# Optimization experiments

Hardware: AMD Instinct MI355X
Metric: run time of the kernel (lower is better)

## Reference

```python
import jax, jax.numpy as jnp
import numpy as np

B, C, M, K, V, D, H, A, L, HF = 2, 128, 4, 4, 64, 1024, 16, 64, 4, 2048
E = M + K
EPS = 1e-5
THETA = 10000.0


def _rmsnorm(x, w):
    return x * jax.lax.rsqrt(jnp.mean(x * x, -1, keepdims=True) + EPS) * w


def _l2norm(x):
    n = jnp.sqrt(jnp.sum(x * x, -1, keepdims=True))
    return x / jnp.maximum(n, EPS)


def _rope(x, cos, sin):
    x1, x2 = jnp.split(x, 2, axis=-1)
    return jnp.concatenate([x1 * cos + x2 * sin, -x1 * sin + x2 * cos], -1)


def _forward(x_input, dec_w1, dec_w2, pos_emb, Wqkv, Wo, Wup, Wdown, attn_norm_w, ffn_norm_w, doc):
    b = x_input.shape[0]
    c = x_input.shape[1] // M
    # decoder_w1 then 'b (c m) (k v) -> b c k (m v)', decoder_w2, pos emb
    x = jnp.einsum('bsd,od->bso', x_input, dec_w1)
    x = x.reshape(b, c, M, K, V).transpose(0, 1, 3, 2, 4).reshape(b, c, K, M * V)
    x = jnp.einsum('bcku,du->bckd', x, dec_w2) + pos_emb
    # decoder_include_original_token: prepend original m tokens per block
    x = jnp.concatenate([x_input.reshape(b, c, M, D), x], axis=2).reshape(b, c * E, D)
    s = c * E
    # mask_mod (decoder_global_original_attn): (causal & kv%e<k & same_doc) | same_block
    idx = jnp.arange(s)
    blk = idx // E
    docs = doc[:, blk]  # [b, s]
    doc_m = docs[:, :, None] == docs[:, None, :]
    causal = blk[:, None] >= blk[None, :]
    kv_ok = (idx % E) < K
    same = blk[:, None] == blk[None, :]
    mask = (causal[None] & kv_ok[None, None, :] & doc_m) | same[None]  # [b, s, s]
    # rotary tables (applied post head-split, dim A)
    inv_freq = (1.0 / THETA) ** (jnp.arange(0, A, 2) / A)
    freqs = jnp.arange(s)[:, None] * inv_freq[None, :]
    cos, sin = jnp.cos(freqs), jnp.sin(freqs)  # [s, A/2]
    scale = 1.0 / jnp.sqrt(jnp.float32(A))
    neg = jnp.float32(-1e30)

    def heads(t):
        return t.reshape(b, s, H, A).transpose(0, 2, 1, 3)

    for li in range(L):
        xn = _rmsnorm(x, attn_norm_w[li])
        qkv = jnp.einsum('bsd,od->bso', xn, Wqkv[li])
        q, k, v = jnp.split(qkv, 3, axis=-1)
        q, k, v = heads(q), heads(k), heads(v)
        q, k = _l2norm(q), _l2norm(k)  # qk_norm
        q, k = _rope(q, cos, sin), _rope(k, cos, sin)
        scores = jnp.einsum('bhqa,bhka->bhqk', q, k) * scale
        scores = jnp.where(mask[:, None], scores, neg)
        probs = jax.nn.softmax(scores, axis=-1)
        attn = jnp.einsum('bhqk,bhka->bhqa', probs, v)
        attn = attn.transpose(0, 2, 1, 3).reshape(b, s, D)
        x1_in = jnp.einsum('bsd,od->bso', attn, Wo[li]) + x
        xf = _rmsnorm(x1_in, ffn_norm_w[li])
        up = jnp.einsum('bsd,od->bso', xf, Wup[li])
        u1, u2 = jnp.split(up, 2, axis=-1)
        x = jnp.einsum('bsh,dh->bsd', jax.nn.silu(u1) * u2, Wdown[li]) + x1_in
    # 'b (c e) d -> (b c) e d' then drop original tokens
    return x.reshape(b * c, E, D)[:, M:]


def setup_inputs() -> dict:
    key = jax.random.key(0)
    ks = jax.random.split(key, 10)
    sc = 0.02
    return {
        'x_input': jax.random.normal(ks[0], (B, C * M, D), jnp.float32),
        'doc': jnp.sort(jax.random.randint(ks[1], (B, C), 0, 4), axis=-1),
        'dec_w1': jax.random.normal(ks[2], (K * V, D), jnp.float32) * sc,
        'dec_w2': jax.random.normal(ks[3], (D, M * V), jnp.float32) * sc,
        'pos_emb': jax.random.normal(ks[4], (1, 1, K, D), jnp.float32) * sc,
        'Wqkv': jax.random.normal(ks[5], (L, 3 * D, D), jnp.float32) * sc,
        'Wo': jax.random.normal(ks[6], (L, D, D), jnp.float32) * sc,
        'Wup': jax.random.normal(ks[7], (L, 2 * HF, D), jnp.float32) * sc,
        'Wdown': jax.random.normal(ks[8], (L, D, HF), jnp.float32) * sc,
        'attn_norm_w': jnp.ones((L, D), jnp.float32),
        'ffn_norm_w': jnp.ones((L, D), jnp.float32),
    }


def reference(x_input, doc, dec_w1, dec_w2, pos_emb, Wqkv, Wo, Wup, Wdown, attn_norm_w, ffn_norm_w):
    return _forward(x_input, dec_w1, dec_w2, pos_emb, Wqkv, Wo, Wup, Wdown, attn_norm_w, ffn_norm_w, doc)
```

## Files before the change

kernel.cpp:

```cpp
#include <hip/hip_runtime.h>
#include <hip/hip_bf16.h>

typedef __bf16 bf16;
typedef __bf16 bf16x8 __attribute__((ext_vector_type(8)));
typedef __bf16 bf16x4 __attribute__((ext_vector_type(4)));
typedef float  f32x4  __attribute__((ext_vector_type(4)));

#define MFMA16(a, b, c) __builtin_amdgcn_mfma_f32_16x16x32_bf16(a, b, c, 0, 0, 0)

template <int EPI, int AF32, int BF32, int TM, int TN, int SK = 1>
__global__ __launch_bounds__(256 * SK) void gemm_bt(
    const void* __restrict__ Av, const void* __restrict__ Bv,
    const float* __restrict__ Res, void* __restrict__ Out,
    int Ntot, int Ktot, int lda)
{
    constexpr int PA = TM / 64, PB = TN / 64;
    constexpr int WN = (TN == 128) ? ((TM == 128) ? 2 : 4) : 2;
    constexpr int WM = 4 / WN;
    constexpr int I = TM / (WM * 16), J = TN / (WN * 16);
    __shared__ __align__(16) bf16 As[2][SK][TM][40];
    __shared__ __align__(16) bf16 Bs[2][SK][TN][40];
    static_assert(SK == 1 || sizeof(As) >= TM * TN * 4, "combine buffer fits in As");
    const int tid  = threadIdx.x;
    const int grp  = (SK > 1) ? (tid >> 8) : 0;
    const int t8   = tid & 255;
    const int wave = t8 >> 6, lane = tid & 63;
    const int quad = lane >> 4, l16 = lane & 15;
    const int wm = wave / WN, wn = wave % WN;
    const int rowW = wm * (TM / WM), colW = wn * (TN / WN);
    const int rowBase = blockIdx.y * TM, colBase = blockIdx.x * TN;

    f32x4 acc[I][J];
    const f32x4 z4 = {0.f, 0.f, 0.f, 0.f};
#pragma unroll
    for (int i = 0; i < I; i++)
#pragma unroll
        for (int j = 0; j < J; j++) acc[i][j] = z4;

    float4 rAf[PA][2]; bf16x8 rAb[PA];
    float4 rBf[PB][2]; bf16x8 rBb[PB];

    auto loadTile = [&](int kt) {
#pragma unroll
        for (int p = 0; p < PA; p++) {
            int ch = p * 256 + t8, r = ch >> 2, c8 = (ch & 3) << 3;
            if (AF32) {
                const float* s = (const float*)Av + (size_t)(rowBase + r) * lda + kt + c8;
                rAf[p][0] = *(const float4*)s; rAf[p][1] = *(const float4*)(s + 4);
            } else {
                rAb[p] = *(const bf16x8*)((const bf16*)Av + (size_t)(rowBase + r) * lda + kt + c8);
            }
        }
#pragma unroll
        for (int p = 0; p < PB; p++) {
            int ch = p * 256 + t8, r = ch >> 2, c8 = (ch & 3) << 3;
            if (BF32) {
                const float* s = (const float*)Bv + (size_t)(colBase + r) * Ktot + kt + c8;
                rBf[p][0] = *(const float4*)s; rBf[p][1] = *(const float4*)(s + 4);
            } else {
                rBb[p] = *(const bf16x8*)((const bf16*)Bv + (size_t)(colBase + r) * Ktot + kt + c8);
            }
        }
    };
    auto storeTile = [&](int buf) {
#pragma unroll
        for (int p = 0; p < PA; p++) {
            int ch = p * 256 + t8, r = ch >> 2, c8 = (ch & 3) << 3;
            bf16x8 t;
            if (AF32) {
                t[0]=(bf16)rAf[p][0].x; t[1]=(bf16)rAf[p][0].y; t[2]=(bf16)rAf[p][0].z; t[3]=(bf16)rAf[p][0].w;
                t[4]=(bf16)rAf[p][1].x; t[5]=(bf16)rAf[p][1].y; t[6]=(bf16)rAf[p][1].z; t[7]=(bf16)rAf[p][1].w;
            } else t = rAb[p];
            *(bf16x8*)&As[buf][grp][r][c8] = t;
        }
#pragma unroll
        for (int p = 0; p < PB; p++) {
            int ch = p * 256 + t8, r = ch >> 2, c8 = (ch & 3) << 3;
            bf16x8 t;
            if (BF32) {
                t[0]=(bf16)rBf[p][0].x; t[1]=(bf16)rBf[p][0].y; t[2]=(bf16)rBf[p][0].z; t[3]=(bf16)rBf[p][0].w;
                t[4]=(bf16)rBf[p][1].x; t[5]=(bf16)rBf[p][1].y; t[6]=(bf16)rBf[p][1].z; t[7]=(bf16)rBf[p][1].w;
            } else t = rBb[p];
            *(bf16x8*)&Bs[buf][grp][r][c8] = t;
        }
    };

    const int Kgrp  = Ktot / SK;
    const int kbase = grp * Kgrp;
    loadTile(kbase);
    storeTile(0);
    __syncthreads();
    const int nk = Kgrp >> 5;
    for (int k = 0; k < nk; k++) {
        const bool more = (k + 1) < nk;
        if (more) loadTile(kbase + ((k + 1) << 5));
        const int buf = k & 1;
        bf16x8 af[I], bfr[J];
#pragma unroll
        for (int i = 0; i < I; i++)
            af[i] = *(const bf16x8*)&As[buf][grp][rowW + i * 16 + l16][quad * 8];
#pragma unroll
        for (int j = 0; j < J; j++)
            bfr[j] = *(const bf16x8*)&Bs[buf][grp][colW + j * 16 + l16][quad * 8];
#pragma unroll
        for (int i = 0; i < I; i++)
#pragma unroll
            for (int j = 0; j < J; j++)
                acc[i][j] = MFMA16(af[i], bfr[j], acc[i][j]);
        if (more) { storeTile(buf ^ 1); __syncthreads(); }
    }

    if (SK == 2) {
        __syncthreads();
        float* red = (float*)&As[0][0][0][0];
        if (grp == 1) {
#pragma unroll
            for (int i = 0; i < I; i++)
#pragma unroll
                for (int j = 0; j < J; j++)
#pragma unroll
                    for (int r = 0; r < 4; r++)
                        red[(rowW + i * 16 + quad * 4 + r) * TN +
                            (colW + j * 16 + l16)] = acc[i][j][r];
        }
        __syncthreads();
        if (grp != 0) return;
#pragma unroll
        for (int i = 0; i < I; i++)
#pragma unroll
            for (int j = 0; j < J; j++)
#pragma unroll
                for (int r = 0; r < 4; r++)
                    acc[i][j][r] += red[(rowW + i * 16 + quad * 4 + r) * TN +
                                        (colW + j * 16 + l16)];
    }

#pragma unroll
    for (int i = 0; i < I; i++) {
        int row0 = rowBase + rowW + i * 16 + quad * 4;
#pragma unroll
        for (int j = 0; j < J; j++) {
            int col = colBase + colW + j * 16 + l16;
#pragma unroll
            for (int r = 0; r < 4; r++) {
                size_t off = (size_t)(row0 + r) * Ntot + col;
                float v = acc[i][j][r];
                if (EPI == 0)      ((bf16*)Out)[off]  = (bf16)v;
                else if (EPI == 1) ((float*)Out)[off] = v + Res[off];
                else               ((float*)Out)[off] = v;
            }
        }
    }
}

__global__ __launch_bounds__(512) void gemm_up_swiglu(
    const bf16* __restrict__ A, const float* __restrict__ B,
    bf16* __restrict__ Out)
{
    __shared__ __align__(16) bf16 Smem[2][2][256][40];
    const int tid  = threadIdx.x;
    const int grp  = tid >> 8, t8 = tid & 255;
    const int wave = t8 >> 6, lane = tid & 63;
    const int quad = lane >> 4, l16 = lane & 15;
    const int wm = wave >> 1, wn = wave & 1;
    const int rowBase = blockIdx.y * 128, cb = blockIdx.x;

    f32x4 acc[4][4];
    const f32x4 z4 = {0.f, 0.f, 0.f, 0.f};
#pragma unroll
    for (int i = 0; i < 4; i++)
#pragma unroll
        for (int j = 0; j < 4; j++) acc[i][j] = z4;

    bf16x8 rA[2]; float4 rB[2][2];
    auto loadTile = [&](int kt) {
#pragma unroll
        for (int p = 0; p < 2; p++) {
            int ch = p * 256 + t8, r = ch >> 2, c8 = (ch & 3) << 3;
            rA[p] = *(const bf16x8*)(A + (size_t)(rowBase + r) * 1024 + kt + c8);
            int brow = (r >> 6) * 2048 + cb * 64 + (r & 63);
            const float* s = B + (size_t)brow * 1024 + kt + c8;
            rB[p][0] = *(const float4*)s; rB[p][1] = *(const float4*)(s + 4);
        }
    };
    auto storeTile = [&](int buf) {
#pragma unroll
        for (int p = 0; p < 2; p++) {
            int ch = p * 256 + t8, r = ch >> 2, c8 = (ch & 3) << 3;
            *(bf16x8*)&Smem[buf][grp][r][c8] = rA[p];
            bf16x8 t;
            t[0]=(bf16)rB[p][0].x; t[1]=(bf16)rB[p][0].y; t[2]=(bf16)rB[p][0].z; t[3]=(bf16)rB[p][0].w;
            t[4]=(bf16)rB[p][1].x; t[5]=(bf16)rB[p][1].y; t[6]=(bf16)rB[p][1].z; t[7]=(bf16)rB[p][1].w;
            *(bf16x8*)&Smem[buf][grp][128 + r][c8] = t;
        }
    };

    const int kbase = grp * 512;
    loadTile(kbase);
    storeTile(0);
    __syncthreads();
    for (int k = 0; k < 16; k++) {
        const bool more = k < 15;
        if (more) loadTile(kbase + ((k + 1) << 5));
        const int buf = k & 1;
        bf16x8 af[4], bfr[4];
#pragma unroll
        for (int i = 0; i < 4; i++)
            af[i] = *(const bf16x8*)&Smem[buf][grp][wm * 64 + i * 16 + l16][quad * 8];
#pragma unroll
        for (int j = 0; j < 4; j++) {
            int brow = (j < 2) ? (wn * 32 + j * 16) : (64 + wn * 32 + (j - 2) * 16);
            bfr[j] = *(const bf16x8*)&Smem[buf][grp][128 + brow + l16][quad * 8];
        }
#pragma unroll
        for (int i = 0; i < 4; i++)
#pragma unroll
            for (int j = 0; j < 4; j++)
                acc[i][j] = MFMA16(af[i], bfr[j], acc[i][j]);
        if (more) { storeTile(buf ^ 1); __syncthreads(); }
    }

    __syncthreads();
    float* red = (float*)&Smem[0][0][0][0];
    if (grp == 1) {
#pragma unroll
        for (int i = 0; i < 4; i++)
#pragma unroll
            for (int j = 0; j < 4; j++) {
                int brow = ((j < 2) ? (wn * 32 + j * 16)
                                    : (64 + wn * 32 + (j - 2) * 16)) + l16;
#pragma unroll
                for (int r = 0; r < 4; r++)
                    red[(wm * 64 + i * 16 + quad * 4 + r) * 128 + brow] = acc[i][j][r];
            }
    }
    __syncthreads();
    if (grp != 0) return;
#pragma unroll
    for (int i = 0; i < 4; i++)
#pragma unroll
        for (int j = 0; j < 4; j++) {
            int brow = ((j < 2) ? (wn * 32 + j * 16)
                                : (64 + wn * 32 + (j - 2) * 16)) + l16;
#pragma unroll
            for (int r = 0; r < 4; r++)
                acc[i][j][r] += red[(wm * 64 + i * 16 + quad * 4 + r) * 128 + brow];
        }

#pragma unroll
    for (int i = 0; i < 4; i++) {
        int row0 = rowBase + wm * 64 + i * 16 + quad * 4;
#pragma unroll
        for (int jj = 0; jj < 2; jj++) {
            int col = cb * 64 + wn * 32 + jj * 16 + l16;
#pragma unroll
            for (int r = 0; r < 4; r++) {
                float u1 = acc[i][jj][r], u2 = acc[i][jj + 2][r];
                float g = u1 / (1.f + __expf(-u1));
                Out[(size_t)(row0 + r) * 2048 + col] = (bf16)(g * u2);
            }
        }
    }
}

__global__ __launch_bounds__(256) void rmsnorm_k(
    const float* __restrict__ X, const float* __restrict__ W,
    bf16* __restrict__ Out)
{
    const int row = blockIdx.x, tid = threadIdx.x;
    const float4 xv = *(const float4*)(X + (size_t)row * 1024 + tid * 4);
    float ss = xv.x * xv.x + xv.y * xv.y + xv.z * xv.z + xv.w * xv.w;
#pragma unroll
    for (int m = 1; m < 64; m <<= 1) ss += __shfl_xor(ss, m);
    __shared__ float red[4];
    if ((tid & 63) == 0) red[tid >> 6] = ss;
    __syncthreads();
    float tot = red[0] + red[1] + red[2] + red[3];
    float sc = rsqrtf(tot * (1.0f / 1024.0f) + 1e-5f);
    const float4 wv = *(const float4*)(W + tid * 4);
    bf16x4 o;
    o[0] = (bf16)(xv.x * sc * wv.x);
    o[1] = (bf16)(xv.y * sc * wv.y);
    o[2] = (bf16)(xv.z * sc * wv.z);
    o[3] = (bf16)(xv.w * sc * wv.w);
    *(bf16x4*)(Out + (size_t)row * 1024 + tid * 4) = o;
}

__global__ __launch_bounds__(256) void ropetab_k(float* __restrict__ tab)
{
    int i = blockIdx.x * 256 + threadIdx.x;
    int s = i >> 5, j = i & 31;
    float f = (float)s * __expf(-(float)j * 0.2878231366242557f);
    tab[i * 2]     = cosf(f);
    tab[i * 2 + 1] = sinf(f);
}

__global__ __launch_bounds__(256) void qkprep_k(
    bf16* __restrict__ qkv, const float* __restrict__ tab)
{
    int wid  = blockIdx.x * 4 + (threadIdx.x >> 6);
    int lane = threadIdx.x & 63;
    int s = wid & 1023, h = (wid >> 10) & 15, b = (wid >> 14) & 1, op = wid >> 15;
    bf16* addr = qkv + ((size_t)(b * 1024 + s)) * 3072 + op * 1024 + h * 64 + lane;
    float v = (float)*addr;
    float ss = v * v;
#pragma unroll
    for (int m = 1; m < 64; m <<= 1) ss += __shfl_xor(ss, m);
    v /= fmaxf(sqrtf(ss), 1e-5f);
    float2 cssn = ((const float2*)tab)[(s << 5) + (lane & 31)];
    float partner = __shfl_xor(v, 32);
    float o = (lane < 32) ? (v * cssn.x + partner * cssn.y)
                          : (v * cssn.x - partner * cssn.y);
    if (op == 0) o *= 0.125f;
    *addr = (bf16)o;
}

__global__ __launch_bounds__(256) void vtrans_k(
    const bf16* __restrict__ qkv, bf16* __restrict__ Vt)
{
    __shared__ __align__(16) bf16 Ls[64][72];
    const int st = blockIdx.x, h = blockIdx.y, b = blockIdx.z;
    const int tid = threadIdx.x;
#pragma unroll
    for (int p = 0; p < 2; p++) {
        int s = p * 32 + (tid >> 3), a0 = (tid & 7) << 3;
        *(bf16x8*)&Ls[s][a0] = *(const bf16x8*)(
            qkv + ((size_t)(b * 1024 + st * 64 + s)) * 3072 + 2048 + h * 64 + a0);
    }
    __syncthreads();
#pragma unroll
    for (int p = 0; p < 2; p++) {
        int a = p * 32 + (tid >> 3), s0 = (tid & 7) << 3;
        bf16x8 v;
#pragma unroll
        for (int j = 0; j < 8; j++) v[j] = Ls[s0 + j][a];
        *(bf16x8*)(Vt + (((size_t)((b * 16 + h) * 64 + a)) << 10) + st * 64 + s0) = v;
    }
}

__global__ __launch_bounds__(256) void attn_k(
    const bf16* __restrict__ qkv, const bf16* __restrict__ Vt,
    const int* __restrict__ doc, bf16* __restrict__ attnb)
{
    const int p = blockIdx.x, h = blockIdx.y, b = blockIdx.z;
    const int tid = threadIdx.x, w = tid >> 6, lane = tid & 63;
    const int quad = lane >> 4, l16 = lane & 15;
    __shared__ __align__(16) bf16 Ks[2][64][72];
    __shared__ __align__(16) bf16 Vs[2][64][72];
    __shared__ __align__(16) bf16 PsT[4][64][20];
    __shared__ int docL[128];
    if (tid < 128) docL[tid] = doc[b * 128 + tid];

    const int g = 4 * p + w;
    const int Tw   = (g + 4) >> 2;
    const int maxT = (4 * p + 7) >> 2;

    const bf16* qp = qkv + ((size_t)(b * 1024 + g * 16 + l16)) * 3072 + h * 64 + quad * 8;
    const bf16x8 qf0 = *(const bf16x8*)qp;
    const bf16x8 qf1 = *(const bf16x8*)(qp + 32);
    const bf16* Kbase = qkv + ((size_t)(b * 1024)) * 3072 + 1024 + h * 64;
    const bf16* Vbase = Vt + (((size_t)((b * 16 + h) * 64)) << 10);

    const f32x4 z4 = {0.f, 0.f, 0.f, 0.f};
    f32x4 O[4] = {z4, z4, z4, z4};
    float lp[4] = {0.f, 0.f, 0.f, 0.f};

    __syncthreads();
    int bq[4], dq[4];
#pragma unroll
    for (int r = 0; r < 4; r++) {
        bq[r] = (g * 16 + quad * 4 + r) >> 3;
        dq[r] = docL[bq[r]];
    }

    bf16x8 rK[2], rV[2];
    auto stageRegs = [&](int kt) {
#pragma unroll
        for (int c = 0; c < 2; c++) {
            int ch = c * 256 + tid, r = ch >> 3, c8 = (ch & 7) << 3;
            rK[c] = *(const bf16x8*)(Kbase + (size_t)(kt * 64 + r) * 3072 + c8);
            rV[c] = *(const bf16x8*)(Vbase + ((size_t)r << 10) + kt * 64 + c8);
        }
    };
    auto stageLDS = [&](int buf) {
#pragma unroll
        for (int c = 0; c < 2; c++) {
            int ch = c * 256 + tid, r = ch >> 3, c8 = (ch & 7) << 3;
            *(bf16x8*)&Ks[buf][r][c8] = rK[c];
            *(bf16x8*)&Vs[buf][r][c8] = rV[c];
        }
    };

    stageRegs(0);
    stageLDS(0);
    __syncthreads();
    for (int kt = 0; kt < maxT; kt++) {
        const bool more = (kt + 1) < maxT;
        if (more) stageRegs(kt + 1);
        const int buf = kt & 1;
        if (kt < Tw) {
            const int k0 = kt * 64;
            f32x4 sf[4];
#pragma unroll
            for (int kg = 0; kg < 4; kg++) {
                const bf16x8 k0f = *(const bf16x8*)&Ks[buf][kg * 16 + l16][quad * 8];
                const bf16x8 k1f = *(const bf16x8*)&Ks[buf][kg * 16 + l16][32 + quad * 8];
                sf[kg] = z4;
                sf[kg] = MFMA16(qf0, k0f, sf[kg]);
                sf[kg] = MFMA16(qf1, k1f, sf[kg]);
            }
            float pvv[4][4];
#pragma unroll
            for (int kg = 0; kg < 4; kg++) {
                int kgi = k0 + kg * 16 + l16;
                int bk  = kgi >> 3;
                int dkv = docL[bk];
                bool kbit = (kgi & 7) < 4;
#pragma unroll
                for (int r = 0; r < 4; r++) {
                    bool ok = (bq[r] == bk) || ((bq[r] >= bk) && kbit && (dq[r] == dkv));
                    float pp = ok ? __expf(sf[kg][r]) : 0.f;
                    pvv[kg][r] = pp;
                    lp[r] += pp;
                }
            }
#pragma unroll
            for (int kg = 0; kg < 4; kg++) {
                bf16x4 t4;
#pragma unroll
                for (int r = 0; r < 4; r++) t4[r] = (bf16)pvv[kg][r];
                *(bf16x4*)&PsT[w][kg * 16 + l16][quad * 4] = t4;
            }
            bf16x8 pa0, pa1;
#pragma unroll
            for (int j = 0; j < 8; j++) {
                pa0[j] = PsT[w][quad * 8 + j][l16];
                pa1[j] = PsT[w][32 + quad * 8 + j][l16];
            }
#pragma unroll
            for (int t = 0; t < 4; t++) {
                const bf16x8 v0f = *(const bf16x8*)&Vs[buf][t * 16 + l16][quad * 8];
                const bf16x8 v1f = *(const bf16x8*)&Vs[buf][t * 16 + l16][32 + quad * 8];
                O[t] = MFMA16(pa0, v0f, O[t]);
                O[t] = MFMA16(pa1, v1f, O[t]);
            }
        }
        if (more) stageLDS(buf ^ 1);
        __syncthreads();
    }

#pragma unroll
    for (int r = 0; r < 4; r++) {
#pragma unroll
        for (int m = 1; m < 16; m <<= 1) lp[r] += __shfl_xor(lp[r], m);
    }

#pragma unroll
    for (int t = 0; t < 4; t++)
#pragma unroll
        for (int r = 0; r < 4; r++) {
            int qg = g * 16 + quad * 4 + r;
            float v = O[t][r] / fmaxf(lp[r], 1e-20f);
            attnb[((size_t)(b * 1024) + qg) * 1024 + h * 64 + t * 16 + l16] = (bf16)v;
        }
}

__global__ __launch_bounds__(256) void permute_k(
    const bf16* __restrict__ t1, bf16* __restrict__ t1p)
{
    int idx = blockIdx.x * 256 + threadIdx.x;
    int u = idx & 255, m = u >> 6, v = u & 63;
    int orow = idx >> 8;
    int k = orow & 3, bc = orow >> 2;
    int b = bc >> 7, c = bc & 127;
    t1p[idx] = t1[((size_t)(b * 512 + c * 4 + m)) * 256 + k * 64 + v];
}

__global__ __launch_bounds__(256) void buildx_k(
    const float* __restrict__ x_input, const float* __restrict__ t2,
    const float* __restrict__ pos_emb, float* __restrict__ xres)
{
    int idx = blockIdx.x * 256 + threadIdx.x;
    int d = idx & 1023, row = idx >> 10;
    int b = row >> 10, rr = row & 1023;
    int c = rr >> 3, e = rr & 7;
    float v;
    if (e < 4)
        v = x_input[((size_t)(b * 512 + c * 4 + e)) * 1024 + d];
    else
        v = t2[((size_t)(b * 512 + c * 4 + (e - 4))) * 1024 + d] +
            pos_emb[(e - 4) * 1024 + d];
    xres[idx] = v;
}

__global__ __launch_bounds__(256) void finalout_k(
    const float* __restrict__ xres, float* __restrict__ out)
{
    int idx = blockIdx.x * 256 + threadIdx.x;
    int d = idx & 1023, t = idx >> 10;
    int kk = t & 3, bc = t >> 2;
    int b = bc >> 7, c = bc & 127;
    out[idx] = xres[((size_t)(b * 1024 + c * 8 + 4 + kk)) * 1024 + d];
}

extern "C" void kernel_launch(void* const* d_in, const int* in_sizes, int n_in,
                              void* d_out, int out_size, void* d_ws, size_t ws_size,
                              hipStream_t stream)
{
    const float* x_input = (const float*)d_in[0];
    const int*   doc     = (const int*)d_in[1];
    const float* dec_w1  = (const float*)d_in[2];
    const float* dec_w2  = (const float*)d_in[3];
    const float* pos_emb = (const float*)d_in[4];
    const float* Wqkv    = (const float*)d_in[5];
    const float* Wo      = (const float*)d_in[6];
    const float* Wup     = (const float*)d_in[7];
    const float* Wdown   = (const float*)d_in[8];
    const float* anw     = (const float*)d_in[9];
    const float* fnw     = (const float*)d_in[10];
    float* out = (float*)d_out;

    char* w = (char*)d_ws;
    float* xres  = (float*)(w);
    bf16*  attnb = (bf16*)(w + (8u << 20));
    bf16*  t1    = (bf16*)(w + (8u << 20));
    bf16*  t1p   = (bf16*)(w + (8u << 20) + (512u << 10));
    bf16*  Vt    = (bf16*)(w + (12u << 20));
    bf16*  xn2   = (bf16*)(w + (12u << 20));
    bf16*  qkv   = (bf16*)(w + (16u << 20));
    float* t2    = (float*)(w + (16u << 20));
    float* x1res = (float*)(w + (16u << 20));
    bf16*  hg    = (bf16*)(w + (24u << 20));
    bf16*  xn1   = (bf16*)(w + (28u << 20));
    float* rtab  = out;

    ropetab_k<<<128, 256, 0, stream>>>(rtab);
    gemm_bt<0, 1, 1, 64, 64><<<dim3(4, 16), 256, 0, stream>>>(
        x_input, dec_w1, nullptr, t1, 256, 1024, 1024);
    permute_k<<<1024, 256, 0, stream>>>(t1, t1p);
    gemm_bt<2, 0, 1, 64, 64><<<dim3(16, 16), 256, 0, stream>>>(
        t1p, dec_w2, nullptr, t2, 1024, 256, 256);
    buildx_k<<<8192, 256, 0, stream>>>(x_input, t2, pos_emb, xres);

    for (int li = 0; li < 4; ++li) {
        rmsnorm_k<<<2048, 256, 0, stream>>>(xres, anw + li * 1024, xn1);
        gemm_bt<0, 0, 1, 128, 128><<<dim3(24, 16), 256, 0, stream>>>(
            xn1, Wqkv + (size_t)li * 3072 * 1024, nullptr, qkv, 3072, 1024, 1024);
        qkprep_k<<<16384, 256, 0, stream>>>(qkv, rtab);
        vtrans_k<<<dim3(16, 16, 2), 256, 0, stream>>>(qkv, Vt);
        attn_k<<<dim3(16, 16, 2), 256, 0, stream>>>(qkv, Vt, doc, attnb);
        gemm_bt<1, 0, 1, 64, 64, 2><<<dim3(16, 32), 512, 0, stream>>>(
            attnb, Wo + (size_t)li * 1024 * 1024, xres, x1res, 1024, 1024, 1024);
        rmsnorm_k<<<2048, 256, 0, stream>>>(x1res, fnw + li * 1024, xn2);
        gemm_up_swiglu<<<dim3(32, 16), 512, 0, stream>>>(
            xn2, Wup + (size_t)li * 4096 * 1024, hg);
        gemm_bt<1, 0, 1, 64, 64, 2><<<dim3(16, 32), 512, 0, stream>>>(
            hg, Wdown + (size_t)li * 1024 * 2048, x1res, xres, 1024, 2048, 2048);
    }

    finalout_k<<<4096, 256, 0, stream>>>(xres, out);
}
```

Measured before the change: 885.5 us.

## Split attention over key chunks with atomic accumulation and a separate normalize pass

Attention is split-K: each query block's key range is cut into chunks of up to four 64-key tiles, spreading 40 blocks per head instead of 16 so the causal triangle load balances better. Partial unnormalized outputs and row sums are accumulated with fp32 atomics into a workspace that vtrans_k zeroes. A new attn_norm kernel divides and converts to bf16. It adds atomic traffic, an extra kernel launch, and workspace buffer reshuffling, with the row-sum buffer placed inside the output array.

New measurement: 898.8 us. About the same (+1.5%).

```diff
diff --git a/kernel.cpp b/kernel.cpp
--- a/kernel.cpp
+++ b/kernel.cpp
@@ -316,11 +316,20 @@
 }
 
 __global__ __launch_bounds__(256) void vtrans_k(
-    const bf16* __restrict__ qkv, bf16* __restrict__ Vt)
+    const bf16* __restrict__ qkv, bf16* __restrict__ Vt,
+    float* __restrict__ Oacc, float* __restrict__ lacc)
 {
     __shared__ __align__(16) bf16 Ls[64][72];
     const int st = blockIdx.x, h = blockIdx.y, b = blockIdx.z;
     const int tid = threadIdx.x;
+
+    int gi = ((b * 16 + h) * 16 + st) * 256 + tid;
+    float* Oz = Oacc + (size_t)gi * 16;
+    const float4 zf = {0.f, 0.f, 0.f, 0.f};
+    *(float4*)Oz = zf; *(float4*)(Oz + 4) = zf;
+    *(float4*)(Oz + 8) = zf; *(float4*)(Oz + 12) = zf;
+    if (gi < 32768) lacc[gi] = 0.f;
+
 #pragma unroll
     for (int p = 0; p < 2; p++) {
         int s = p * 32 + (tid >> 3), a0 = (tid & 7) << 3;
@@ -338,23 +347,34 @@
     }
 }
 
-__global__ __launch_bounds__(256) void attn_k(
+__global__ __launch_bounds__(256) void attn_part(
     const bf16* __restrict__ qkv, const bf16* __restrict__ Vt,
-    const int* __restrict__ doc, bf16* __restrict__ attnb)
-{
-    const int p = blockIdx.x, h = blockIdx.y, b = blockIdx.z;
+    const int* __restrict__ doc,
+    float* __restrict__ Oacc, float* __restrict__ lacc)
+{
+    const int h = blockIdx.y, b = blockIdx.z;
     const int tid = threadIdx.x, w = tid >> 6, lane = tid & 63;
     const int quad = lane >> 4, l16 = lane & 15;
-    __shared__ __align__(16) bf16 Ks[2][64][72];
-    __shared__ __align__(16) bf16 Vs[2][64][72];
-    __shared__ __align__(16) bf16 PsT[4][64][20];
-    __shared__ int docL[128];
+
+    __shared__ __align__(16) char smraw[47616];
+    bf16 (*Ks)[64][72]  = (bf16(*)[64][72])(smraw);
+    bf16 (*Vs)[64][72]  = (bf16(*)[64][72])(smraw + 18432);
+    bf16 (*PsT)[64][20] = (bf16(*)[64][20])(smraw + 36864);
+    int* docL           = (int*)(smraw + 47104);
+
     if (tid < 128) docL[tid] = doc[b * 128 + tid];
 
+    int xr = blockIdx.x, p = 0, c = 0;
+    for (;;) {
+        int ch = (p >> 2) + 1;
+        if (xr < ch) { c = xr; break; }
+        xr -= ch; p++;
+    }
+    const int ck0 = c * 4;
+    const int T   = p + 1;
+    const int ck1 = (ck0 + 4 < T) ? (ck0 + 4) : T;
+
     const int g = 4 * p + w;
-    const int Tw   = (g + 4) >> 2;
-    const int maxT = (4 * p + 7) >> 2;
-
     const bf16* qp = qkv + ((size_t)(b * 1024 + g * 16 + l16)) * 3072 + h * 64 + quad * 8;
     const bf16x8 qf0 = *(const bf16x8*)qp;
     const bf16x8 qf1 = *(const bf16x8*)(qp + 32);
@@ -376,93 +396,116 @@
     bf16x8 rK[2], rV[2];
     auto stageRegs = [&](int kt) {
 #pragma unroll
-        for (int c = 0; c < 2; c++) {
-            int ch = c * 256 + tid, r = ch >> 3, c8 = (ch & 7) << 3;
-            rK[c] = *(const bf16x8*)(Kbase + (size_t)(kt * 64 + r) * 3072 + c8);
-            rV[c] = *(const bf16x8*)(Vbase + ((size_t)r << 10) + kt * 64 + c8);
+        for (int cc = 0; cc < 2; cc++) {
+            int ch = cc * 256 + tid, r = ch >> 3, c8 = (ch & 7) << 3;
+            rK[cc] = *(const bf16x8*)(Kbase + (size_t)(kt * 64 + r) * 3072 + c8);
+            rV[cc] = *(const bf16x8*)(Vbase + ((size_t)r << 10) + kt * 64 + c8);
         }
     };
     auto stageLDS = [&](int buf) {
 #pragma unroll
-        for (int c = 0; c < 2; c++) {
-            int ch = c * 256 + tid, r = ch >> 3, c8 = (ch & 7) << 3;
-            *(bf16x8*)&Ks[buf][r][c8] = rK[c];
-            *(bf16x8*)&Vs[buf][r][c8] = rV[c];
+        for (int cc = 0; cc < 2; cc++) {
+            int ch = cc * 256 + tid, r = ch >> 3, c8 = (ch & 7) << 3;
+            *(bf16x8*)&Ks[buf][r][c8] = rK[cc];
+            *(bf16x8*)&Vs[buf][r][c8] = rV[cc];
         }
     };
 
-    stageRegs(0);
+    stageRegs(ck0);
     stageLDS(0);
     __syncthreads();
-    for (int kt = 0; kt < maxT; kt++) {
-        const bool more = (kt + 1) < maxT;
+    for (int kt = ck0; kt < ck1; kt++) {
+        const bool more = (kt + 1) < ck1;
         if (more) stageRegs(kt + 1);
-        const int buf = kt & 1;
-        if (kt < Tw) {
-            const int k0 = kt * 64;
-            f32x4 sf[4];
-#pragma unroll
-            for (int kg = 0; kg < 4; kg++) {
-                const bf16x8 k0f = *(const bf16x8*)&Ks[buf][kg * 16 + l16][quad * 8];
-                const bf16x8 k1f = *(const bf16x8*)&Ks[buf][kg * 16 + l16][32 + quad * 8];
-                sf[kg] = z4;
-                sf[kg] = MFMA16(qf0, k0f, sf[kg]);
-                sf[kg] = MFMA16(qf1, k1f, sf[kg]);
+        const int buf = (kt - ck0) & 1;
+        const int k0 = kt * 64;
+        f32x4 sf[4];
+#pragma unroll
+        for (int kg = 0; kg < 4; kg++) {
+            const bf16x8 k0f = *(const bf16x8*)&Ks[buf][kg * 16 + l16][quad * 8];
+            const bf16x8 k1f = *(const bf16x8*)&Ks[buf][kg * 16 + l16][32 + quad * 8];
+            sf[kg] = z4;
+            sf[kg] = MFMA16(qf0, k0f, sf[kg]);
+            sf[kg] = MFMA16(qf1, k1f, sf[kg]);
+        }
+        float pvv[4][4];
+#pragma unroll
+        for (int kg = 0; kg < 4; kg++) {
+            int kgi = k0 + kg * 16 + l16;
+            int bk  = kgi >> 3;
+            int dkv = docL[bk];
+            bool kbit = (kgi & 7) < 4;
+#pragma unroll
+            for (int r = 0; r < 4; r++) {
+                bool ok = (bq[r] == bk) || ((bq[r] >= bk) && kbit && (dq[r] == dkv));
+                float pp = ok ? __expf(sf[kg][r]) : 0.f;
+                pvv[kg][r] = pp;
+                lp[r] += pp;
             }
-            float pvv[4][4];
-#pragma unroll
-            for (int kg = 0; kg < 4; kg++) {
-                int kgi = k0 + kg * 16 + l16;
-                int bk  = kgi >> 3;
-                int dkv = docL[bk];
-                bool kbit = (kgi & 7) < 4;
-#pragma unroll
-                for (int r = 0; r < 4; r++) {
-                    bool ok = (bq[r] == bk) || ((bq[r] >= bk) && kbit && (dq[r] == dkv));
-                    float pp = ok ? __expf(sf[kg][r]) : 0.f;
-                    pvv[kg][r] = pp;
-                    lp[r] += pp;
-                }
-            }
-#pragma unroll
-            for (int kg = 0; kg < 4; kg++) {
-                bf16x4 t4;
-#pragma unroll
-                for (int r = 0; r < 4; r++) t4[r] = (bf16)pvv[kg][r];
-                *(bf16x4*)&PsT[w][kg * 16 + l16][quad * 4] = t4;
-            }
-            bf16x8 pa0, pa1;
-#pragma unroll
-            for (int j = 0; j < 8; j++) {
-                pa0[j] = PsT[w][quad * 8 + j][l16];
-                pa1[j] = PsT[w][32 + quad * 8 + j][l16];
-            }
-#pragma unroll
-            for (int t = 0; t < 4; t++) {
-                const bf16x8 v0f = *(const bf16x8*)&Vs[buf][t * 16 + l16][quad * 8];
-                const bf16x8 v1f = *(const bf16x8*)&Vs[buf][t * 16 + l16][32 + quad * 8];
-                O[t] = MFMA16(pa0, v0f, O[t]);
-                O[t] = MFMA16(pa1, v1f, O[t]);
-            }
+        }
+#pragma unroll
+        for (int kg = 0; kg < 4; kg++) {
+            bf16x4 t4;
+#pragma unroll
+            for (int r = 0; r < 4; r++) t4[r] = (bf16)pvv[kg][r];
+            *(bf16x4*)&PsT[w][kg * 16 + l16][quad * 4] = t4;
+        }
+        bf16x8 pa0, pa1;
+#pragma unroll
+        for (int j = 0; j < 8; j++) {
+            pa0[j] = PsT[w][quad * 8 + j][l16];
+            pa1[j] = PsT[w][32 + quad * 8 + j][l16];
+        }
+#pragma unroll
+        for (int t = 0; t < 4; t++) {
+            const bf16x8 v0f = *(const bf16x8*)&Vs[buf][t * 16 + l16][quad * 8];
+            const bf16x8 v1f = *(const bf16x8*)&Vs[buf][t * 16 + l16][32 + quad * 8];
+            O[t] = MFMA16(pa0, v0f, O[t]);
+            O[t] = MFMA16(pa1, v1f, O[t]);
         }
         if (more) stageLDS(buf ^ 1);
         __syncthreads();
     }
 
+    float* Osc = (float*)smraw + w * 1024;
+#pragma unroll
+    for (int t = 0; t < 4; t++)
+#pragma unroll
+        for (int r = 0; r < 4; r++)
+            Osc[(quad * 4 + r) * 64 + t * 16 + l16] = O[t][r];
+
 #pragma unroll
     for (int r = 0; r < 4; r++) {
 #pragma unroll
         for (int m = 1; m < 16; m <<= 1) lp[r] += __shfl_xor(lp[r], m);
     }
-
-#pragma unroll
-    for (int t = 0; t < 4; t++)
-#pragma unroll
-        for (int r = 0; r < 4; r++) {
-            int qg = g * 16 + quad * 4 + r;
-            float v = O[t][r] / fmaxf(lp[r], 1e-20f);
-            attnb[((size_t)(b * 1024) + qg) * 1024 + h * 64 + t * 16 + l16] = (bf16)v;
-        }
+    const size_t rowb = (size_t)(b * 1024 + g * 16);
+    if (l16 < 4) {
+        float myl = (l16 == 0) ? lp[0] : (l16 == 1) ? lp[1] : (l16 == 2) ? lp[2] : lp[3];
+        atomicAdd(&lacc[(rowb + quad * 4 + l16) * 16 + h], myl);
+    }
+
+    float* Obase = Oacc + rowb * 1024 + h * 64;
+#pragma unroll
+    for (int i = 0; i < 16; i++)
+        atomicAdd(&Obase[(size_t)i * 1024 + lane], Osc[i * 64 + lane]);
+}
+
+__global__ __launch_bounds__(256) void attn_norm(
+    const float* __restrict__ Oacc, const float* __restrict__ lacc,
+    bf16* __restrict__ attnb)
+{
+    int i8 = (blockIdx.x * 256 + threadIdx.x) * 8;
+    int row = i8 >> 10, d0 = i8 & 1023;
+    float inv = 1.0f / fmaxf(lacc[row * 16 + (d0 >> 6)], 1e-20f);
+    const float4 a = *(const float4*)(Oacc + i8);
+    const float4 bvv = *(const float4*)(Oacc + i8 + 4);
+    bf16x8 o;
+    o[0] = (bf16)(a.x * inv); o[1] = (bf16)(a.y * inv);
+    o[2] = (bf16)(a.z * inv); o[3] = (bf16)(a.w * inv);
+    o[4] = (bf16)(bvv.x * inv); o[5] = (bf16)(bvv.y * inv);
+    o[6] = (bf16)(bvv.z * inv); o[7] = (bf16)(bvv.w * inv);
+    *(bf16x8*)(attnb + i8) = o;
 }
 
 __global__ __launch_bounds__(256) void permute_k(
@@ -522,17 +565,19 @@
 
     char* w = (char*)d_ws;
     float* xres  = (float*)(w);
-    bf16*  attnb = (bf16*)(w + (8u << 20));
+    bf16*  xn1   = (bf16*)(w + (8u << 20));
+    bf16*  xn2   = (bf16*)(w + (8u << 20));
+    float* Oacc  = (float*)(w + (8u << 20));
     bf16*  t1    = (bf16*)(w + (8u << 20));
     bf16*  t1p   = (bf16*)(w + (8u << 20) + (512u << 10));
-    bf16*  Vt    = (bf16*)(w + (12u << 20));
-    bf16*  xn2   = (bf16*)(w + (12u << 20));
     bf16*  qkv   = (bf16*)(w + (16u << 20));
     float* t2    = (float*)(w + (16u << 20));
     float* x1res = (float*)(w + (16u << 20));
+    bf16*  attnb = (bf16*)(w + (24u << 20));
     bf16*  hg    = (bf16*)(w + (24u << 20));
-    bf16*  xn1   = (bf16*)(w + (28u << 20));
+    bf16*  Vt    = (bf16*)(w + (28u << 20));
     float* rtab  = out;
+    float* lacc  = out + 131072;
 
     ropetab_k<<<128, 256, 0, stream>>>(rtab);
     gemm_bt<0, 1, 1, 64, 64><<<dim3(4, 16), 256, 0, stream>>>(
@@ -547,8 +592,9 @@
         gemm_bt<0, 0, 1, 128, 128><<<dim3(24, 16), 256, 0, stream>>>(
             xn1, Wqkv + (size_t)li * 3072 * 1024, nullptr, qkv, 3072, 1024, 1024);
         qkprep_k<<<16384, 256, 0, stream>>>(qkv, rtab);
-        vtrans_k<<<dim3(16, 16, 2), 256, 0, stream>>>(qkv, Vt);
-        attn_k<<<dim3(16, 16, 2), 256, 0, stream>>>(qkv, Vt, doc, attnb);
+        vtrans_k<<<dim3(16, 16, 2), 256, 0, stream>>>(qkv, Vt, Oacc, lacc);
+        attn_part<<<dim3(40, 16, 2), 256, 0, stream>>>(qkv, Vt, doc, Oacc, lacc);
+        attn_norm<<<1024, 256, 0, stream>>>(Oacc, lacc, attnb);
         gemm_bt<1, 0, 1, 64, 64, 2><<<dim3(16, 32), 512, 0, stream>>>(
             attnb, Wo + (size_t)li * 1024 * 1024, xres, x1res, 1024, 1024, 1024);
         rmsnorm_k<<<2048, 256, 0, stream>>>(x1res, fnw + li * 1024, xn2);
```
